# Kernel optimization log

Measured on AMD Instinct MI355X. Metric: run time of the kernel, lower is better.

Reference implementation:

```python
import jax, jax.numpy as jnp
import numpy as np

HEADS = 16
DIM_HEAD = 64
NUM_W = 4  # num_adaptive_weights
SCALE = DIM_HEAD ** -0.5


def setup_inputs() -> dict:
    key = jax.random.key(0)
    k0, k1, k2, k3 = jax.random.split(key, 4)
    b, n, dim = 2, 2048, 1024
    dim_inner = HEADS * DIM_HEAD  # 1024
    x = jax.random.normal(k0, (b, n, dim), jnp.float32)
    # Linear weights stored as (in, out); torch Linear(in,out,bias=False) computes x @ W.T
    Wqkv = jax.random.normal(k1, (dim, dim_inner * 3 * NUM_W), jnp.float32) * (dim ** -0.5)
    Wg = jax.random.normal(k2, (dim, NUM_W), jnp.float32) * (dim ** -0.5)
    Wout = jax.random.normal(k3, (dim_inner, dim * NUM_W), jnp.float32) * (dim_inner ** -0.5)
    mask = jnp.ones((b, n), dtype=bool)
    return {"x": x, "Wqkv": Wqkv, "Wg": Wg, "Wout": Wout, "mask": mask}


def reference(x, Wqkv, Wg, Wout, mask):
    b, n, dim = x.shape
    # to_qkv: packed last dim order is (qkv, h, d, w) per Rearrange 'b n (qkv h d w) -> qkv b h n d w'
    qkv = (x @ Wqkv).reshape(b, n, 3, HEADS, DIM_HEAD, NUM_W)
    qkv = jnp.transpose(qkv, (2, 0, 3, 1, 4, 5))  # [3, b, h, n, d, w]
    # adaptive gates: softmax over the w adaptive weights
    gates = jax.nn.softmax(x @ Wg, axis=-1)  # [b, n, w]
    # gated sum over adaptive-weight axis
    qkv = jnp.einsum('qbhndw,bnw->qbhnd', qkv, gates)
    q, k, v = qkv[0] * SCALE, qkv[1], qkv[2]
    sim = jnp.einsum('bhid,bhjd->bhij', q, k)  # [b, h, n, n]
    sim = jnp.where(mask[:, None, None, :], sim, jnp.finfo(sim.dtype).min)
    attn = jax.nn.softmax(sim, axis=-1)
    out = jnp.einsum('bhij,bhjd->bhid', attn, v)  # [b, h, n, d]
    out = out.transpose(0, 2, 1, 3).reshape(b, n, HEADS * DIM_HEAD)  # 'b h n d -> b n (h d)'
    out = (out @ Wout).reshape(b, n, dim, NUM_W)  # 'b n (d w) -> b n d w'
    # gated sum over w for the output projection
    return jnp.einsum('bndw,bnw->bnd', out, gates)
```

## Files before the change

### kernel.cpp

```cpp
#include <hip/hip_runtime.h>
#include <hip/hip_bf16.h>

#define M_TOT 4096
#define DIM_  1024
#define KP    4096
#define NC1   3072
#define NC2   1024

typedef unsigned short u16;
typedef unsigned int u32;
typedef unsigned long long u64;
typedef short bf16x8 __attribute__((ext_vector_type(8)));
typedef float f32x4 __attribute__((ext_vector_type(4)));

#define QSCALE 0.18033688011112042f
#define EXPOFF 20.0f

static __device__ __forceinline__ u16 f2bf(float f) {
    union { float f; u32 u; } v; v.f = f;
    u32 u = v.u;
    u += 0x7fffu + ((u >> 16) & 1u);
    return (u16)(u >> 16);
}
static __device__ __forceinline__ float bf2f(u16 h) {
    union { u32 u; float f; } v; v.u = ((u32)h) << 16; return v.f;
}

static __device__ __forceinline__ void gld_lds16(const u16* g, u16* l) {
    __builtin_amdgcn_global_load_lds(
        (__attribute__((address_space(1))) void*)(u64)g,
        (__attribute__((address_space(3))) void*)(u32)(u64)l,
        16, 0, 0);
}

__global__ __launch_bounds__(256) void gates_expand_kernel(const float* __restrict__ x,
                                                           const float* __restrict__ Wg,
                                                           float* __restrict__ gates,
                                                           u16* __restrict__ outA) {
    const int wid = threadIdx.x >> 6, lane = threadIdx.x & 63;
    const int m = blockIdx.x * 4 + wid;
    const float* xr = x + (size_t)m * DIM_;
    float a0 = 0.f, a1 = 0.f, a2 = 0.f, a3 = 0.f;
    for (int i = 0; i < DIM_ / 64; ++i) {
        int k = i * 64 + lane;
        float xv = xr[k];
        float4 wg = ((const float4*)Wg)[k];
        a0 += xv * wg.x; a1 += xv * wg.y; a2 += xv * wg.z; a3 += xv * wg.w;
    }
    for (int s = 1; s < 64; s <<= 1) {
        a0 += __shfl_xor(a0, s); a1 += __shfl_xor(a1, s);
        a2 += __shfl_xor(a2, s); a3 += __shfl_xor(a3, s);
    }
    float mx = fmaxf(fmaxf(a0, a1), fmaxf(a2, a3));
    float e0 = __expf(a0 - mx), e1 = __expf(a1 - mx), e2 = __expf(a2 - mx), e3 = __expf(a3 - mx);
    float inv = 1.0f / (e0 + e1 + e2 + e3);
    float g0 = e0 * inv, g1 = e1 * inv, g2 = e2 * inv, g3 = e3 * inv;
    if (lane == 0) ((float4*)gates)[m] = make_float4(g0, g1, g2, g3);
    ushort4* out4 = (ushort4*)outA;
    for (int i = 0; i < DIM_ / 64; ++i) {
        int k = i * 64 + lane;
        float val = xr[k];
        ushort4 o;
        o.x = f2bf(val * g0); o.y = f2bf(val * g1); o.z = f2bf(val * g2); o.w = f2bf(val * g3);
        out4[(size_t)m * 1024 + k] = o;
    }
}

__global__ __launch_bounds__(256) void expand_kernel(const u16* __restrict__ in,
                                                     const float* __restrict__ gates,
                                                     u16* __restrict__ outA) {
    size_t idx = (size_t)blockIdx.x * 256 + threadIdx.x;
    int m = (int)(idx >> 10);
    float val = bf2f(in[idx]);
    float4 g = ((const float4*)gates)[m];
    ushort4 o;
    o.x = f2bf(val * g.x); o.y = f2bf(val * g.y); o.z = f2bf(val * g.z); o.w = f2bf(val * g.w);
    ((ushort4*)outA)[idx] = o;
}

__global__ __launch_bounds__(256) void bprep_kernel(const float* __restrict__ src,
                                                    u16* __restrict__ dst,
                                                    int R, int Cg) {
    __shared__ u16 lds[64 * 68];
    const int t = threadIdx.x;
    const int cg0 = blockIdx.x * 16, k0 = blockIdx.y * 64;
    const float4* s4 = (const float4*)src;
    for (int i = 0; i < 4; ++i) {
        int f = i * 256 + t;
        int kl = f >> 4, f4 = f & 15;
        float4 v = s4[(size_t)(k0 + kl) * Cg + cg0 + f4];
        ushort4 o; o.x = f2bf(v.x); o.y = f2bf(v.y); o.z = f2bf(v.z); o.w = f2bf(v.w);
        *(ushort4*)&lds[kl * 68 + f4 * 4] = o;
    }
    __syncthreads();
    ushort4* d4 = (ushort4*)dst;
    for (int i = 0; i < 4; ++i) {
        int j = i * 256 + t;
        int cgl = j >> 6, kl = j & 63;
        d4[(size_t)(cg0 + cgl) * R + k0 + kl] = *(ushort4*)&lds[kl * 68 + cgl * 4];
    }
}

template <int EPI>
__global__ __launch_bounds__(256) void gemm_kernel(const u16* __restrict__ A,
                                                   const u16* __restrict__ Bm,
                                                   void* __restrict__ out0,
                                                   u16* __restrict__ kbuf,
                                                   u16* __restrict__ vbuf) {
    __shared__ u16 lA[128 * 64];
    __shared__ u16 lB[128 * 64];
    const int t = threadIdx.x;
    const int lane = t & 63, wid = t >> 6;
    const int wm = wid >> 1, wn = wid & 1;
    const int l15 = lane & 15, quad = lane >> 4;
    const int n0 = blockIdx.x * 128, m0 = blockIdx.y * 128;
    const int srow = lane >> 3, scol = (lane & 7) * 8;
    const u16* gA = A + (size_t)(m0 + wid * 32 + srow) * KP + scol;
    const u16* gB = Bm + (size_t)(n0 + wid * 32 + srow) * KP + scol;
    u16* lAw = &lA[wid * 2048];
    u16* lBw = &lB[wid * 2048];
    f32x4 acc[4][4] = {};
    for (int k0 = 0; k0 < KP; k0 += 64) {
        for (int i = 0; i < 4; ++i)
            gld_lds16(gA + (size_t)i * 8 * KP + k0, lAw + i * 512);
        for (int i = 0; i < 4; ++i)
            gld_lds16(gB + (size_t)i * 8 * KP + k0, lBw + i * 512);
        __syncthreads();
        for (int ks = 0; ks < 2; ++ks) {
            bf16x8 af[4], bfr[4];
            for (int mt = 0; mt < 4; ++mt)
                af[mt] = *(const bf16x8*)&lA[(wm * 64 + mt * 16 + l15) * 64 + ks * 32 + quad * 8];
            for (int nt = 0; nt < 4; ++nt)
                bfr[nt] = *(const bf16x8*)&lB[(wn * 64 + nt * 16 + l15) * 64 + ks * 32 + quad * 8];
            for (int mt = 0; mt < 4; ++mt)
                for (int nt = 0; nt < 4; ++nt)
                    acc[mt][nt] = __builtin_amdgcn_mfma_f32_16x16x32_bf16(af[mt], bfr[nt], acc[mt][nt], 0, 0, 0);
        }
        __syncthreads();
    }
    if (EPI == 1) {
        const int qkv = n0 >> 10;
        const int base_hd = n0 & 1023;
        u16* qbuf = (u16*)out0;
        for (int mt = 0; mt < 4; ++mt) {
            int mrow = m0 + wm * 64 + mt * 16 + quad * 4;
            for (int nt = 0; nt < 4; ++nt) {
                int hd = base_hd + wn * 64 + nt * 16 + l15;
                int h = hd >> 6, d = hd & 63;
                for (int r = 0; r < 4; ++r) {
                    int m = mrow + r;
                    int b = m >> 11, n = m & 2047;
                    int bh = b * 16 + h;
                    float val = acc[mt][nt][r];
                    if (qkv == 0)
                        qbuf[((size_t)bh * 2048 + n) * 64 + d] = f2bf(val * QSCALE);
                    else if (qkv == 1)
                        kbuf[((size_t)bh * 2048 + n) * 64 + d] = f2bf(val);
                    else
                        vbuf[((size_t)bh * 64 + d) * 2048 + n] = f2bf(val);
                }
            }
        }
    } else {
        float* outf = (float*)out0;
        for (int mt = 0; mt < 4; ++mt) {
            int mrow = m0 + wm * 64 + mt * 16 + quad * 4;
            for (int nt = 0; nt < 4; ++nt) {
                int col = n0 + wn * 64 + nt * 16 + l15;
                for (int r = 0; r < 4; ++r)
                    outf[(size_t)(mrow + r) * NC2 + col] = acc[mt][nt][r];
            }
        }
    }
}

__global__ __launch_bounds__(256) void attn_kernel(const u16* __restrict__ qbuf,
                                                   const u16* __restrict__ kbuf,
                                                   const u16* __restrict__ vbuf,
                                                   u16* __restrict__ outbuf) {
    __shared__ u16 lK[64 * 64];
    __shared__ u16 lV[64 * 64];
    __shared__ u16 lP[8 * 16 * 72];
    const int t = threadIdx.x, lane = t & 63, wq = t >> 6;
    const int l15 = lane & 15, quad = lane >> 4;
    const int bh = blockIdx.y, q0 = blockIdx.x * 128;
    const u16* Q = qbuf + (size_t)bh * 2048 * 64;
    const u16* K = kbuf + (size_t)bh * 2048 * 64;
    const u16* V = vbuf + (size_t)bh * 64 * 2048;
    bf16x8 qf[2][2];
    for (int mt = 0; mt < 2; ++mt)
        for (int ks = 0; ks < 2; ++ks)
            qf[mt][ks] = *(const bf16x8*)&Q[(size_t)(q0 + wq * 32 + mt * 16 + l15) * 64 + ks * 32 + quad * 8];
    f32x4 Oa[2][4] = {};
    float lacc[2] = {0.f, 0.f};
    const int srow = lane >> 3, scol = (lane & 7) * 8;
    const u16* gK = K + (size_t)(wq * 16 + srow) * 64 + scol;
    const u16* gV = V + (size_t)(wq * 16 + srow) * 2048 + scol;
    u16* lKw = &lK[wq * 16 * 64];
    u16* lVw = &lV[wq * 16 * 64];
    u16* lPw = &lP[wq * 2 * 16 * 72];
    for (int kt = 0; kt < 32; ++kt) {
        const int nk = kt * 64;
        __syncthreads();
        gld_lds16(gK + (size_t)nk * 64, lKw);
        gld_lds16(gK + (size_t)nk * 64 + 8 * 64, lKw + 512);
        gld_lds16(gV + nk, lVw);
        gld_lds16(gV + nk + 8 * 2048, lVw + 512);
        __syncthreads();
        f32x4 S[2][4] = {};
        for (int ks = 0; ks < 2; ++ks)
            for (int nt = 0; nt < 4; ++nt) {
                bf16x8 kf = *(const bf16x8*)&lK[(nt * 16 + l15) * 64 + ks * 32 + quad * 8];
                S[0][nt] = __builtin_amdgcn_mfma_f32_16x16x32_bf16(kf, qf[0][ks], S[0][nt], 0, 0, 0);
                S[1][nt] = __builtin_amdgcn_mfma_f32_16x16x32_bf16(kf, qf[1][ks], S[1][nt], 0, 0, 0);
            }
        for (int mt = 0; mt < 2; ++mt) {
            u16* lPm = lPw + mt * (16 * 72);
            for (int nt = 0; nt < 4; ++nt) {
                float p0 = __builtin_amdgcn_exp2f(S[mt][nt][0] - EXPOFF);
                float p1 = __builtin_amdgcn_exp2f(S[mt][nt][1] - EXPOFF);
                float p2 = __builtin_amdgcn_exp2f(S[mt][nt][2] - EXPOFF);
                float p3 = __builtin_amdgcn_exp2f(S[mt][nt][3] - EXPOFF);
                lacc[mt] += (p0 + p1) + (p2 + p3);
                uint2 pk;
                pk.x = (u32)f2bf(p0) | ((u32)f2bf(p1) << 16);
                pk.y = (u32)f2bf(p2) | ((u32)f2bf(p3) << 16);
                *(uint2*)&lPm[l15 * 72 + nt * 16 + quad * 4] = pk;
            }
        }
        asm volatile("s_waitcnt lgkmcnt(0)" ::: "memory");
        for (int ks = 0; ks < 2; ++ks) {
            bf16x8 p0 = *(const bf16x8*)&lPw[0 * (16 * 72) + l15 * 72 + ks * 32 + quad * 8];
            bf16x8 p1 = *(const bf16x8*)&lPw[1 * (16 * 72) + l15 * 72 + ks * 32 + quad * 8];
            for (int dt = 0; dt < 4; ++dt) {
                bf16x8 vf = *(const bf16x8*)&lV[(dt * 16 + l15) * 64 + ks * 32 + quad * 8];
                Oa[0][dt] = __builtin_amdgcn_mfma_f32_16x16x32_bf16(p0, vf, Oa[0][dt], 0, 0, 0);
                Oa[1][dt] = __builtin_amdgcn_mfma_f32_16x16x32_bf16(p1, vf, Oa[1][dt], 0, 0, 0);
            }
        }
    }
    for (int mt = 0; mt < 2; ++mt) {
        lacc[mt] += __shfl_xor(lacc[mt], 16);
        lacc[mt] += __shfl_xor(lacc[mt], 32);
    }
    const int b = bh >> 4, h = bh & 15;
    for (int mt = 0; mt < 2; ++mt) {
        for (int r = 0; r < 4; ++r) {
            int n = q0 + wq * 32 + mt * 16 + quad * 4 + r;
            float invl = 1.0f / __shfl(lacc[mt], quad * 4 + r);
            size_t rowbase = ((size_t)b * 2048 + n) * 1024 + h * 64;
            for (int dt = 0; dt < 4; ++dt)
                outbuf[rowbase + dt * 16 + l15] = f2bf(Oa[mt][dt][r] * invl);
        }
    }
}

extern "C" void kernel_launch(void* const* d_in, const int* in_sizes, int n_in,
                              void* d_out, int out_size, void* d_ws, size_t ws_size,
                              hipStream_t stream) {
    const float* x    = (const float*)d_in[0];
    const float* Wqkv = (const float*)d_in[1];
    const float* Wg   = (const float*)d_in[2];
    const float* Wout = (const float*)d_in[3];

    char* ws = (char*)d_ws;
    size_t off = 0;
    float* gates = (float*)(ws + off); off += (size_t)1 << 16;
    u16* Aexp = (u16*)(ws + off);      off += (size_t)M_TOT * KP * 2;
    char* regB = ws + off;             off += (size_t)NC1 * KP * 2;
    u16* B1 = (u16*)regB;
    u16* attn_out = (u16*)regB;
    u16* B2 = (u16*)(regB + (size_t)M_TOT * NC2 * 2);
    u16* qbuf = (u16*)(ws + off); off += (size_t)32 * 2048 * 64 * 2;
    u16* kbuf = (u16*)(ws + off); off += (size_t)32 * 2048 * 64 * 2;
    u16* vbuf = (u16*)(ws + off); off += (size_t)32 * 2048 * 64 * 2;

    hipLaunchKernelGGL(gates_expand_kernel, dim3(1024), dim3(256), 0, stream,
                       x, Wg, gates, Aexp);
    hipLaunchKernelGGL(bprep_kernel, dim3(192, 16), dim3(256), 0, stream,
                       Wqkv, B1, 1024, 3072);
    hipLaunchKernelGGL(gemm_kernel<1>, dim3(24, 32), dim3(256), 0, stream,
                       Aexp, B1, (void*)qbuf, kbuf, vbuf);
    hipLaunchKernelGGL(bprep_kernel, dim3(64, 16), dim3(256), 0, stream,
                       Wout, B2, 1024, 1024);
    hipLaunchKernelGGL(attn_kernel, dim3(16, 32), dim3(256), 0, stream,
                       qbuf, kbuf, vbuf, attn_out);
    hipLaunchKernelGGL(expand_kernel, dim3(16384), dim3(256), 0, stream,
                       attn_out, gates, Aexp);
    hipLaunchKernelGGL(gemm_kernel<2>, dim3(8, 32), dim3(256), 0, stream,
                       Aexp, B2, d_out, (u16*)nullptr, (u16*)nullptr);
}
```

Baseline: 425.6 us.

## Swizzle LDS tiles in GEMM and attention, split GEMM2 into narrower tiles

Applies an XOR swizzle to the 16-byte column chunks written into LDS by global_load_lds and read back for MFMA fragments in both GEMMs and the attention K/V tiles, to remove LDS bank conflicts on row-strided reads. The output GEMM now uses 128x64 tiles with twice as many blocks (512 vs 256) to fill more CUs. The V epilogue of the QKV GEMM writes four contiguous bf16 values as one vector store. Narrower GEMM2 tiles lower arithmetic intensity per block and raise total A-matrix reloads.

```diff
diff --git a/kernel.cpp b/kernel.cpp
--- a/kernel.cpp
+++ b/kernel.cpp
@@ -32,6 +32,8 @@
         (__attribute__((address_space(3))) void*)(u32)(u64)l,
         16, 0, 0);
 }
+
+#define SWZ_SCOL(lane) ((((lane) & 7) ^ (((lane) >> 3) & 7)) * 8)
 
 __global__ __launch_bounds__(256) void gates_expand_kernel(const float* __restrict__ x,
                                                            const float* __restrict__ Wg,
@@ -101,20 +103,20 @@
     }
 }
 
-template <int EPI>
-__global__ __launch_bounds__(256) void gemm_kernel(const u16* __restrict__ A,
-                                                   const u16* __restrict__ Bm,
-                                                   void* __restrict__ out0,
-                                                   u16* __restrict__ kbuf,
-                                                   u16* __restrict__ vbuf) {
+__global__ __launch_bounds__(256) void gemm1_kernel(const u16* __restrict__ A,
+                                                    const u16* __restrict__ Bm,
+                                                    u16* __restrict__ qbuf,
+                                                    u16* __restrict__ kbuf,
+                                                    u16* __restrict__ vbuf) {
     __shared__ u16 lA[128 * 64];
     __shared__ u16 lB[128 * 64];
     const int t = threadIdx.x;
     const int lane = t & 63, wid = t >> 6;
     const int wm = wid >> 1, wn = wid & 1;
     const int l15 = lane & 15, quad = lane >> 4;
+    const int sx = l15 & 7;
     const int n0 = blockIdx.x * 128, m0 = blockIdx.y * 128;
-    const int srow = lane >> 3, scol = (lane & 7) * 8;
+    const int srow = lane >> 3, scol = SWZ_SCOL(lane);
     const u16* gA = A + (size_t)(m0 + wid * 32 + srow) * KP + scol;
     const u16* gB = Bm + (size_t)(n0 + wid * 32 + srow) * KP + scol;
     u16* lAw = &lA[wid * 2048];
@@ -127,49 +129,86 @@
             gld_lds16(gB + (size_t)i * 8 * KP + k0, lBw + i * 512);
         __syncthreads();
         for (int ks = 0; ks < 2; ++ks) {
+            const int co = ((ks * 4 + quad) ^ sx) * 8;
             bf16x8 af[4], bfr[4];
             for (int mt = 0; mt < 4; ++mt)
-                af[mt] = *(const bf16x8*)&lA[(wm * 64 + mt * 16 + l15) * 64 + ks * 32 + quad * 8];
+                af[mt] = *(const bf16x8*)&lA[(wm * 64 + mt * 16 + l15) * 64 + co];
             for (int nt = 0; nt < 4; ++nt)
-                bfr[nt] = *(const bf16x8*)&lB[(wn * 64 + nt * 16 + l15) * 64 + ks * 32 + quad * 8];
+                bfr[nt] = *(const bf16x8*)&lB[(wn * 64 + nt * 16 + l15) * 64 + co];
             for (int mt = 0; mt < 4; ++mt)
                 for (int nt = 0; nt < 4; ++nt)
                     acc[mt][nt] = __builtin_amdgcn_mfma_f32_16x16x32_bf16(af[mt], bfr[nt], acc[mt][nt], 0, 0, 0);
         }
         __syncthreads();
     }
-    if (EPI == 1) {
-        const int qkv = n0 >> 10;
-        const int base_hd = n0 & 1023;
-        u16* qbuf = (u16*)out0;
-        for (int mt = 0; mt < 4; ++mt) {
-            int mrow = m0 + wm * 64 + mt * 16 + quad * 4;
-            for (int nt = 0; nt < 4; ++nt) {
-                int hd = base_hd + wn * 64 + nt * 16 + l15;
-                int h = hd >> 6, d = hd & 63;
-                for (int r = 0; r < 4; ++r) {
-                    int m = mrow + r;
-                    int b = m >> 11, n = m & 2047;
-                    int bh = b * 16 + h;
-                    float val = acc[mt][nt][r];
-                    if (qkv == 0)
-                        qbuf[((size_t)bh * 2048 + n) * 64 + d] = f2bf(val * QSCALE);
-                    else if (qkv == 1)
-                        kbuf[((size_t)bh * 2048 + n) * 64 + d] = f2bf(val);
-                    else
-                        vbuf[((size_t)bh * 64 + d) * 2048 + n] = f2bf(val);
-                }
+    const int qkv = n0 >> 10;
+    const int base_hd = n0 & 1023;
+    for (int mt = 0; mt < 4; ++mt) {
+        int mrow = m0 + wm * 64 + mt * 16 + quad * 4;
+        int b = mrow >> 11, n = mrow & 2047;
+        int bh0 = b * 16;
+        for (int nt = 0; nt < 4; ++nt) {
+            int hd = base_hd + wn * 64 + nt * 16 + l15;
+            int h = hd >> 6, d = hd & 63;
+            int bh = bh0 + h;
+            if (qkv == 0) {
+                for (int r = 0; r < 4; ++r)
+                    qbuf[((size_t)bh * 2048 + n + r) * 64 + d] = f2bf(acc[mt][nt][r] * QSCALE);
+            } else if (qkv == 1) {
+                for (int r = 0; r < 4; ++r)
+                    kbuf[((size_t)bh * 2048 + n + r) * 64 + d] = f2bf(acc[mt][nt][r]);
+            } else {
+                ushort4 o;
+                o.x = f2bf(acc[mt][nt][0]); o.y = f2bf(acc[mt][nt][1]);
+                o.z = f2bf(acc[mt][nt][2]); o.w = f2bf(acc[mt][nt][3]);
+                *(ushort4*)&vbuf[((size_t)bh * 64 + d) * 2048 + n] = o;
             }
         }
-    } else {
-        float* outf = (float*)out0;
-        for (int mt = 0; mt < 4; ++mt) {
-            int mrow = m0 + wm * 64 + mt * 16 + quad * 4;
-            for (int nt = 0; nt < 4; ++nt) {
-                int col = n0 + wn * 64 + nt * 16 + l15;
-                for (int r = 0; r < 4; ++r)
-                    outf[(size_t)(mrow + r) * NC2 + col] = acc[mt][nt][r];
-            }
+    }
+}
+
+__global__ __launch_bounds__(256) void gemm2_kernel(const u16* __restrict__ A,
+                                                    const u16* __restrict__ Bm,
+                                                    float* __restrict__ outf) {
+    __shared__ u16 lA[128 * 64];
+    __shared__ u16 lB[64 * 64];
+    const int t = threadIdx.x;
+    const int lane = t & 63, wid = t >> 6;
+    const int wm = wid >> 1, wn = wid & 1;
+    const int l15 = lane & 15, quad = lane >> 4;
+    const int sx = l15 & 7;
+    const int n0 = blockIdx.x * 64, m0 = blockIdx.y * 128;
+    const int srow = lane >> 3, scol = SWZ_SCOL(lane);
+    const u16* gA = A + (size_t)(m0 + wid * 32 + srow) * KP + scol;
+    const u16* gB = Bm + (size_t)(n0 + wid * 16 + srow) * KP + scol;
+    u16* lAw = &lA[wid * 2048];
+    u16* lBw = &lB[wid * 1024];
+    f32x4 acc[4][2] = {};
+    for (int k0 = 0; k0 < KP; k0 += 64) {
+        for (int i = 0; i < 4; ++i)
+            gld_lds16(gA + (size_t)i * 8 * KP + k0, lAw + i * 512);
+        for (int i = 0; i < 2; ++i)
+            gld_lds16(gB + (size_t)i * 8 * KP + k0, lBw + i * 512);
+        __syncthreads();
+        for (int ks = 0; ks < 2; ++ks) {
+            const int co = ((ks * 4 + quad) ^ sx) * 8;
+            bf16x8 af[4], bfr[2];
+            for (int mt = 0; mt < 4; ++mt)
+                af[mt] = *(const bf16x8*)&lA[(wm * 64 + mt * 16 + l15) * 64 + co];
+            for (int nt = 0; nt < 2; ++nt)
+                bfr[nt] = *(const bf16x8*)&lB[(wn * 32 + nt * 16 + l15) * 64 + co];
+            for (int mt = 0; mt < 4; ++mt)
+                for (int nt = 0; nt < 2; ++nt)
+                    acc[mt][nt] = __builtin_amdgcn_mfma_f32_16x16x32_bf16(af[mt], bfr[nt], acc[mt][nt], 0, 0, 0);
+        }
+        __syncthreads();
+    }
+    for (int mt = 0; mt < 4; ++mt) {
+        int mrow = m0 + wm * 64 + mt * 16 + quad * 4;
+        for (int nt = 0; nt < 2; ++nt) {
+            int col = n0 + wn * 32 + nt * 16 + l15;
+            for (int r = 0; r < 4; ++r)
+                outf[(size_t)(mrow + r) * NC2 + col] = acc[mt][nt][r];
         }
     }
 }
@@ -183,6 +222,7 @@
     __shared__ u16 lP[8 * 16 * 72];
     const int t = threadIdx.x, lane = t & 63, wq = t >> 6;
     const int l15 = lane & 15, quad = lane >> 4;
+    const int sx = l15 & 7;
     const int bh = blockIdx.y, q0 = blockIdx.x * 128;
     const u16* Q = qbuf + (size_t)bh * 2048 * 64;
     const u16* K = kbuf + (size_t)bh * 2048 * 64;
@@ -193,7 +233,7 @@
             qf[mt][ks] = *(const bf16x8*)&Q[(size_t)(q0 + wq * 32 + mt * 16 + l15) * 64 + ks * 32 + quad * 8];
     f32x4 Oa[2][4] = {};
     float lacc[2] = {0.f, 0.f};
-    const int srow = lane >> 3, scol = (lane & 7) * 8;
+    const int srow = lane >> 3, scol = SWZ_SCOL(lane);
     const u16* gK = K + (size_t)(wq * 16 + srow) * 64 + scol;
     const u16* gV = V + (size_t)(wq * 16 + srow) * 2048 + scol;
     u16* lKw = &lK[wq * 16 * 64];
@@ -208,12 +248,14 @@
         gld_lds16(gV + nk + 8 * 2048, lVw + 512);
         __syncthreads();
         f32x4 S[2][4] = {};
-        for (int ks = 0; ks < 2; ++ks)
+        for (int ks = 0; ks < 2; ++ks) {
+            const int co = ((ks * 4 + quad) ^ sx) * 8;
             for (int nt = 0; nt < 4; ++nt) {
-                bf16x8 kf = *(const bf16x8*)&lK[(nt * 16 + l15) * 64 + ks * 32 + quad * 8];
+                bf16x8 kf = *(const bf16x8*)&lK[(nt * 16 + l15) * 64 + co];
                 S[0][nt] = __builtin_amdgcn_mfma_f32_16x16x32_bf16(kf, qf[0][ks], S[0][nt], 0, 0, 0);
                 S[1][nt] = __builtin_amdgcn_mfma_f32_16x16x32_bf16(kf, qf[1][ks], S[1][nt], 0, 0, 0);
             }
+        }
         for (int mt = 0; mt < 2; ++mt) {
             u16* lPm = lPw + mt * (16 * 72);
             for (int nt = 0; nt < 4; ++nt) {
@@ -230,10 +272,11 @@
         }
         asm volatile("s_waitcnt lgkmcnt(0)" ::: "memory");
         for (int ks = 0; ks < 2; ++ks) {
+            const int co = ((ks * 4 + quad) ^ sx) * 8;
             bf16x8 p0 = *(const bf16x8*)&lPw[0 * (16 * 72) + l15 * 72 + ks * 32 + quad * 8];
             bf16x8 p1 = *(const bf16x8*)&lPw[1 * (16 * 72) + l15 * 72 + ks * 32 + quad * 8];
             for (int dt = 0; dt < 4; ++dt) {
-                bf16x8 vf = *(const bf16x8*)&lV[(dt * 16 + l15) * 64 + ks * 32 + quad * 8];
+                bf16x8 vf = *(const bf16x8*)&lV[(dt * 16 + l15) * 64 + co];
                 Oa[0][dt] = __builtin_amdgcn_mfma_f32_16x16x32_bf16(p0, vf, Oa[0][dt], 0, 0, 0);
                 Oa[1][dt] = __builtin_amdgcn_mfma_f32_16x16x32_bf16(p1, vf, Oa[1][dt], 0, 0, 0);
             }
@@ -279,14 +322,14 @@
                        x, Wg, gates, Aexp);
     hipLaunchKernelGGL(bprep_kernel, dim3(192, 16), dim3(256), 0, stream,
                        Wqkv, B1, 1024, 3072);
-    hipLaunchKernelGGL(gemm_kernel<1>, dim3(24, 32), dim3(256), 0, stream,
-                       Aexp, B1, (void*)qbuf, kbuf, vbuf);
+    hipLaunchKernelGGL(gemm1_kernel, dim3(24, 32), dim3(256), 0, stream,
+                       Aexp, B1, qbuf, kbuf, vbuf);
     hipLaunchKernelGGL(bprep_kernel, dim3(64, 16), dim3(256), 0, stream,
                        Wout, B2, 1024, 1024);
     hipLaunchKernelGGL(attn_kernel, dim3(16, 32), dim3(256), 0, stream,
                        qbuf, kbuf, vbuf, attn_out);
     hipLaunchKernelGGL(expand_kernel, dim3(16384), dim3(256), 0, stream,
                        attn_out, gates, Aexp);
-    hipLaunchKernelGGL(gemm_kernel<2>, dim3(8, 32), dim3(256), 0, stream,
-                       Aexp, B2, d_out, (u16*)nullptr, (u16*)nullptr);
-}
+    hipLaunchKernelGGL(gemm2_kernel, dim3(16, 32), dim3(256), 0, stream,
+                       Aexp, B2, (float*)d_out);
+}
```

Measured after the change: 395.5 us. 1.08x faster.
